# Optimization experiments

Measured on AMD Instinct MI355X. Metric: run time of the kernel, lower is better.

Reference implementation:

```python
import jax, jax.numpy as jnp
import numpy as np

C_RADIUS = 20.0  # weighted-L1 ball radius from the cvxpy constraint
EPS = 1e-30


def weighted_l1_ball_projection(q, w, c):
    """Euclidean projection of each row of q onto {x : sum_i w_i*|x_i| <= c}, w>=0.
    Closed-form via sorted breakpoints: x_i = sign(q_i)*max(|q_i| - lam*w_i, 0).
    q, w: [B, D].
    """
    aq = jnp.abs(q)
    wa = w * aq                               # w_i |q_i|
    feasible = jnp.sum(wa, axis=-1) <= c      # already inside the ball
    # breakpoint ratios; coords with w==0 are never clipped -> push to the end
    r = jnp.where(w > 0, aq / jnp.maximum(w, EPS), -jnp.inf)
    order = jnp.argsort(-r, axis=-1)
    wa_s = jnp.take_along_axis(wa, order, axis=-1)
    w2_s = jnp.take_along_axis(w * w, order, axis=-1)
    r_s = jnp.take_along_axis(r, order, axis=-1)
    A = jnp.cumsum(wa_s, axis=-1)             # prefix sums over candidate active sets
    B = jnp.cumsum(w2_s, axis=-1)
    lam_k = (A - c) / jnp.maximum(B, EPS)
    valid = r_s > lam_k                       # active-set condition
    k = jnp.sum(valid, axis=-1)               # size of true active set
    idx = jnp.maximum(k - 1, 0)
    lam = jnp.take_along_axis(lam_k, idx[:, None], axis=-1)[:, 0]
    lam = jnp.where(feasible, 0.0, jnp.maximum(lam, 0.0))
    return jnp.sign(q) * jnp.maximum(aq - lam[:, None] * w, 0.0)


def setup_inputs() -> dict:
    key = jax.random.key(0)
    ks = jax.random.split(key, 8)
    state_dim, action_dim, B = 17, 6, 262144
    # scale state so the weighted-L1 constraint is occasionally active
    state = 4.0 * jax.random.normal(ks[0], (B, state_dim), dtype=jnp.float32)
    def lin(kw, kb, fan_out, fan_in):
        bound = 1.0 / np.sqrt(fan_in)
        W = jax.random.uniform(kw, (fan_out, fan_in), jnp.float32, -bound, bound)
        b = jax.random.uniform(kb, (fan_out,), jnp.float32, -bound, bound)
        return W, b
    l1_w, l1_b = lin(ks[1], ks[2], 400, state_dim)
    l2_w, l2_b = lin(ks[3], ks[4], 300, 400)
    l3_w, l3_b = lin(ks[5], ks[6], action_dim, 300)
    return {"state": state, "l1_w": l1_w, "l1_b": l1_b, "l2_w": l2_w,
            "l2_b": l2_b, "l3_w": l3_w, "l3_b": l3_b, "training": 0}


def reference(state, l1_w, l1_b, l2_w, l2_b, l3_w, l3_b, training):
    max_action = 1.0
    a = jax.nn.relu(state @ l1_w.T + l1_b)
    a = jax.nn.relu(a @ l2_w.T + l2_b)
    scaled_a = max_action * jnp.tanh(a @ l3_w.T + l3_b)  # [B, 6]
    # IS_TRAINING path: QP  min 0.5||x||^2 - q^T x  s.t. sum |x_i * s[11+i]| <= 20
    w = jnp.abs(state[:, 11:17])
    return weighted_l1_ball_projection(scaled_a, w, C_RADIUS)
```

## Files before the change

### kernel.cpp

```cpp
#include <hip/hip_runtime.h>
#include <math.h>

typedef _Float16 half2v __attribute__((ext_vector_type(2)));
typedef __fp16 fp16x2 __attribute__((ext_vector_type(2)));
typedef _Float16 half4 __attribute__((ext_vector_type(4)));
typedef _Float16 half8 __attribute__((ext_vector_type(8)));
typedef float floatx4 __attribute__((ext_vector_type(4)));

#define C_RADIUS 20.0f


__global__ void actor_prep(const float* __restrict__ w1, const float* __restrict__ b1,
                           const float* __restrict__ w2, const float* __restrict__ b2,
                           const float* __restrict__ w3, const float* __restrict__ b3,
                           _Float16* __restrict__ ws) {
  int gid = blockIdx.x * 256 + threadIdx.x;
  if (gid >= 19072) return;
  half8 hv;
  _Float16* dst;
  if (gid < 1792) {
    int l = gid & 63, tn = gid >> 6;
    int n = tn * 16 + (l & 15);
    int kc = 8 * (l >> 4);
#pragma unroll
    for (int e = 0; e < 8; ++e) {
      int k = kc + e;
      float v = 0.f;
      if (n < 400) {
        if (k == 0) v = b1[n];
        else if (k <= 17) v = w1[n * 17 + (k - 1)];
      }
      hv[e] = (_Float16)v;
    }
    dst = ws + gid * 8;
  } else if (gid < 1792 + 16640) {
    int g = gid - 1792;
    int l = g & 63, t = g >> 6;
    int ks = t % 13, tn = t / 13;
    int n = tn * 16 + (l & 15);
    int kc = ks * 32 + 8 * (l >> 4);
#pragma unroll
    for (int e = 0; e < 8; ++e) {
      int k = kc + e;
      float v = 0.f;
      if (n < 300) {
        if (k < 400) v = w2[n * 400 + k];
        else if (k == 400) v = b2[n];
      }
      hv[e] = (_Float16)v;
    }
    dst = ws + 14336 + g * 8;
  } else {
    int g = gid - 1792 - 16640;
    int l = g & 63, ks = g >> 6;
    int n = l & 15;
    int kc = ks * 32 + 8 * (l >> 4);
#pragma unroll
    for (int e = 0; e < 8; ++e) {
      int k = kc + e;
      float v = 0.f;
      if (n < 6) {
        if (k < 300) v = w3[n * 300 + k];
        else if (k == 300) v = b3[n];
      }
      hv[e] = (_Float16)v;
    }
    dst = ws + 147456 + g * 8;
  }
  *reinterpret_cast<half8*>(dst) = hv;
}

#define LD1 408
#define LD2 328

#define MFMA32(A, B, C) C = __builtin_amdgcn_mfma_f32_16x16x32_f16(A, B, C, 0, 0, 0)

__device__ __forceinline__ half4 pack4(float v0, float v1, float v2, float v3) {
  fp16x2 a = __builtin_amdgcn_cvt_pkrtz(v0, v1);
  fp16x2 b = __builtin_amdgcn_cvt_pkrtz(v2, v3);
  half2v a2 = __builtin_bit_cast(half2v, a);
  half2v b2 = __builtin_bit_cast(half2v, b);
  return __builtin_shufflevector(a2, b2, 0, 1, 2, 3);
}

__device__ __forceinline__ float fast_tanh(float x) {
  float e = __expf(2.0f * x);
  return 1.0f - 2.0f / (e + 1.0f);
}

__global__ __launch_bounds__(512, 6) void actor_fused(const float* __restrict__ state,
                                                      const _Float16* __restrict__ ws,
                                                      float* __restrict__ out) {
  __shared__ __align__(16) _Float16 aL[64 * LD1 + 16];

  const int tid = threadIdx.x;
  const int lane = tid & 63;
  const int w = tid >> 6;
  const int r15 = lane & 15;
  const int c4 = lane >> 4;
  const int row0 = blockIdx.x * 64;

  for (int i = tid; i < 2048; i += 512) {
    int r = i >> 5, c = i & 31;
    float v = 0.f;
    if (c == 0) v = 1.0f;
    else if (c <= 17) v = state[(row0 + r) * 17 + (c - 1)];
    aL[r * LD1 + c] = (_Float16)v;
  }
  {
    int r = tid >> 3, c = tid & 7;
    aL[r * LD1 + 400 + c] = (c == 0) ? (_Float16)1.0f : (_Float16)0.0f;
  }
  if (tid < 16) aL[64 * LD1 + tid] = (_Float16)0.0f;
  __syncthreads();

  half8 S[4];
#pragma unroll
  for (int m = 0; m < 4; ++m)
    S[m] = *reinterpret_cast<const half8*>(&aL[(16 * m + r15) * LD1 + 8 * c4]);
  __syncthreads();

  {
    const half8* W1f = reinterpret_cast<const half8*>(ws);
#pragma unroll
    for (int t = 0; t < 4; ++t) {
      int tn = w + 8 * t;
      if (tn < 25) {
        half8 aW = W1f[tn * 64 + lane];
        floatx4 acc[4];
#pragma unroll
        for (int m = 0; m < 4; ++m) {
          acc[m] = (floatx4){0.f, 0.f, 0.f, 0.f};
          MFMA32(aW, S[m], acc[m]);
        }
        int n0 = tn * 16 + 4 * c4;
#pragma unroll
        for (int m = 0; m < 4; ++m) {
          half4 hv = pack4(fmaxf(acc[m][0], 0.f), fmaxf(acc[m][1], 0.f),
                           fmaxf(acc[m][2], 0.f), fmaxf(acc[m][3], 0.f));
          *reinterpret_cast<half4*>(&aL[(16 * m + r15) * LD1 + n0]) = hv;
        }
      }
    }
  }
  __syncthreads();

  {
    const half8* W2f = reinterpret_cast<const half8*>(ws + 14336);
    const int nt = (w < 4) ? 3 : 2;
    const int tn0 = (w < 4) ? (w * 3) : (12 + (w - 4) * 2);
    floatx4 acc[4][3];
#pragma unroll
    for (int m = 0; m < 4; ++m)
#pragma unroll
      for (int t = 0; t < 3; ++t) acc[m][t] = (floatx4){0.f, 0.f, 0.f, 0.f};

    half8 bA[3];
#pragma unroll
    for (int t = 0; t < 3; ++t)
      if (t < nt) bA[t] = W2f[((tn0 + t) * 13 + 0) * 64 + lane];

#pragma unroll 1
    for (int ks = 0; ks < 13; ++ks) {
      half8 F[4];
#pragma unroll
      for (int m = 0; m < 4; ++m)
        F[m] = *reinterpret_cast<const half8*>(&aL[(16 * m + r15) * LD1 + ks * 32 + 8 * c4]);
#pragma unroll
      for (int t = 0; t < 3; ++t)
        if (t < nt)
#pragma unroll
          for (int m = 0; m < 4; ++m)
            MFMA32(bA[t], F[m], acc[m][t]);
      if (ks < 12) {
#pragma unroll
        for (int t = 0; t < 3; ++t)
          if (t < nt) bA[t] = W2f[((tn0 + t) * 13 + ks + 1) * 64 + lane];
      }
    }

    __syncthreads();

#pragma unroll
    for (int t = 0; t < 3; ++t)
      if (t < nt) {
        int n0 = (tn0 + t) * 16 + 4 * c4;
#pragma unroll
        for (int m = 0; m < 4; ++m) {
          float v0 = fmaxf(acc[m][t][0], 0.f), v1 = fmaxf(acc[m][t][1], 0.f);
          float v2 = fmaxf(acc[m][t][2], 0.f), v3 = fmaxf(acc[m][t][3], 0.f);
          if (n0 == 300) v0 = 1.0f;
          half4 hv = pack4(v0, v1, v2, v3);
          *reinterpret_cast<half4*>(&aL[(16 * m + r15) * LD2 + n0]) = hv;
        }
      }
  }
  __syncthreads();

  if (w < 4) {
    const half8* W3f = reinterpret_cast<const half8*>(ws + 147456);
    floatx4 za = (floatx4){0.f, 0.f, 0.f, 0.f};
    floatx4 zb = (floatx4){0.f, 0.f, 0.f, 0.f};
    const int row = 16 * w + r15;
#pragma unroll
    for (int ks = 0; ks < 10; ks += 2) {
      half8 F0 = *reinterpret_cast<const half8*>(&aL[row * LD2 + ks * 32 + 8 * c4]);
      half8 F1 = *reinterpret_cast<const half8*>(&aL[row * LD2 + (ks + 1) * 32 + 8 * c4]);
      MFMA32(W3f[ks * 64 + lane], F0, za);
      MFMA32(W3f[(ks + 1) * 64 + lane], F1, zb);
    }
    floatx4 z = za + zb;
    float v4 = __shfl(z[0], r15 + 16, 64);
    float v5 = __shfl(z[1], r15 + 16, 64);
    if (c4 == 0) {
      const int grow = row0 + row;
      float q[6], wv[6], aq[6], wa[6];
      q[0] = fast_tanh(z[0]); q[1] = fast_tanh(z[1]);
      q[2] = fast_tanh(z[2]); q[3] = fast_tanh(z[3]);
      q[4] = fast_tanh(v4);   q[5] = fast_tanh(v5);
      float S2 = 0.f;
#pragma unroll
      for (int i = 0; i < 6; ++i) {
        wv[i] = fabsf(state[grow * 17 + 11 + i]);
        aq[i] = fabsf(q[i]);
        wa[i] = wv[i] * aq[i];
        S2 += wa[i];
      }
      float lam = 0.f;
      if (!(S2 <= C_RADIUS)) {
        float rr[6], w2s[6], was[6];
#pragma unroll
        for (int i = 0; i < 6; ++i) {
          rr[i] = (wv[i] > 0.f) ? (aq[i] / fmaxf(wv[i], 1e-30f)) : -__builtin_inff();
          w2s[i] = wv[i] * wv[i];
          was[i] = wa[i];
        }
#pragma unroll
        for (int p = 0; p < 5; ++p)
#pragma unroll
          for (int j2 = 0; j2 < 5; ++j2)
            if (j2 < 5 - p) {
              if (rr[j2] < rr[j2 + 1]) {
                float t0 = rr[j2];  rr[j2] = rr[j2 + 1];  rr[j2 + 1] = t0;
                float t1 = w2s[j2]; w2s[j2] = w2s[j2 + 1]; w2s[j2 + 1] = t1;
                float t2 = was[j2]; was[j2] = was[j2 + 1]; was[j2 + 1] = t2;
              }
            }
        float A = 0.f, Bc = 0.f;
        float lamk[6];
        int kc = 0;
#pragma unroll
        for (int i = 0; i < 6; ++i) {
          A += was[i];
          Bc += w2s[i];
          lamk[i] = (A - C_RADIUS) / fmaxf(Bc, 1e-30f);
          if (rr[i] > lamk[i]) ++kc;
        }
        int idx = kc - 1;
        if (idx < 0) idx = 0;
        float lsel = lamk[0];
#pragma unroll
        for (int i = 1; i < 6; ++i)
          if (i == idx) lsel = lamk[i];
        lam = fmaxf(lsel, 0.f);
      }
#pragma unroll
      for (int i = 0; i < 6; ++i) {
        float x = fmaxf(aq[i] - lam * wv[i], 0.f);
        out[grow * 6 + i] = copysignf(x, q[i]);
      }
    }
  }
}

extern "C" void kernel_launch(void* const* d_in, const int* in_sizes, int n_in,
                              void* d_out, int out_size, void* d_ws, size_t ws_size,
                              hipStream_t stream) {
  const float* state = (const float*)d_in[0];
  const float* w1 = (const float*)d_in[1];
  const float* b1 = (const float*)d_in[2];
  const float* w2 = (const float*)d_in[3];
  const float* b2 = (const float*)d_in[4];
  const float* w3 = (const float*)d_in[5];
  const float* b3 = (const float*)d_in[6];
  _Float16* ws = (_Float16*)d_ws;
  float* out = (float*)d_out;

  actor_prep<<<75, 256, 0, stream>>>(w1, b1, w2, b2, w3, b3, ws);
  actor_fused<<<4096, 512, 0, stream>>>(state, ws, out);
}
```

Measured before the change: 92.96 us.

## Rebalance layer-2 MFMA work across waves and apply ReLU on packed halves

Layer 2 was split as 3 or 2 column tiles per wave over all 64 rows, which left waves 4-7 with less work. Now each wave handles 5 column tiles over half of the rows (32), so all eight waves issue the same number of MFMAs. This halves the per-wave LDS fragment reads but doubles the weight fragments each wave loads from global memory across the two row halves. The ReLU is also applied after fp16 packing with a packed max instead of four scalar fmaxf calls.

```diff
diff --git a/kernel.cpp b/kernel.cpp
--- a/kernel.cpp
+++ b/kernel.cpp
@@ -83,6 +83,11 @@
   return __builtin_shufflevector(a2, b2, 0, 1, 2, 3);
 }
 
+__device__ __forceinline__ half4 pack4_relu(floatx4 v) {
+  half4 hv = pack4(v[0], v[1], v[2], v[3]);
+  return __builtin_elementwise_max(hv, (half4)(_Float16)0.0f);
+}
+
 __device__ __forceinline__ float fast_tanh(float x) {
   float e = __expf(2.0f * x);
   return 1.0f - 2.0f / (e + 1.0f);
@@ -136,8 +141,7 @@
         int n0 = tn * 16 + 4 * c4;
 #pragma unroll
         for (int m = 0; m < 4; ++m) {
-          half4 hv = pack4(fmaxf(acc[m][0], 0.f), fmaxf(acc[m][1], 0.f),
-                           fmaxf(acc[m][2], 0.f), fmaxf(acc[m][3], 0.f));
+          half4 hv = pack4_relu(acc[m]);
           *reinterpret_cast<half4*>(&aL[(16 * m + r15) * LD1 + n0]) = hv;
         }
       }
@@ -147,53 +151,45 @@
 
   {
     const half8* W2f = reinterpret_cast<const half8*>(ws + 14336);
-    const int nt = (w < 4) ? 3 : 2;
-    const int tn0 = (w < 4) ? (w * 3) : (12 + (w - 4) * 2);
-    floatx4 acc[4][3];
-#pragma unroll
-    for (int m = 0; m < 4; ++m)
-#pragma unroll
-      for (int t = 0; t < 3; ++t) acc[m][t] = (floatx4){0.f, 0.f, 0.f, 0.f};
-
-    half8 bA[3];
-#pragma unroll
-    for (int t = 0; t < 3; ++t)
-      if (t < nt) bA[t] = W2f[((tn0 + t) * 13 + 0) * 64 + lane];
+    const int mh = w >> 2;
+    const int tnb = (w & 3) * 5;
+    floatx4 acc[2][5];
+#pragma unroll
+    for (int mi = 0; mi < 2; ++mi)
+#pragma unroll
+      for (int t = 0; t < 5; ++t) acc[mi][t] = (floatx4){0.f, 0.f, 0.f, 0.f};
+
+    half8 bA[5];
+#pragma unroll
+    for (int t = 0; t < 5; ++t) bA[t] = W2f[((tnb + t) * 13 + 0) * 64 + lane];
 
 #pragma unroll 1
     for (int ks = 0; ks < 13; ++ks) {
-      half8 F[4];
-#pragma unroll
-      for (int m = 0; m < 4; ++m)
-        F[m] = *reinterpret_cast<const half8*>(&aL[(16 * m + r15) * LD1 + ks * 32 + 8 * c4]);
-#pragma unroll
-      for (int t = 0; t < 3; ++t)
-        if (t < nt)
-#pragma unroll
-          for (int m = 0; m < 4; ++m)
-            MFMA32(bA[t], F[m], acc[m][t]);
+      half8 F0 = *reinterpret_cast<const half8*>(&aL[(32 * mh + r15) * LD1 + ks * 32 + 8 * c4]);
+      half8 F1 = *reinterpret_cast<const half8*>(&aL[(32 * mh + 16 + r15) * LD1 + ks * 32 + 8 * c4]);
+#pragma unroll
+      for (int t = 0; t < 5; ++t) {
+        MFMA32(bA[t], F0, acc[0][t]);
+        MFMA32(bA[t], F1, acc[1][t]);
+      }
       if (ks < 12) {
 #pragma unroll
-        for (int t = 0; t < 3; ++t)
-          if (t < nt) bA[t] = W2f[((tn0 + t) * 13 + ks + 1) * 64 + lane];
+        for (int t = 0; t < 5; ++t) bA[t] = W2f[((tnb + t) * 13 + ks + 1) * 64 + lane];
       }
     }
 
     __syncthreads();
 
 #pragma unroll
-    for (int t = 0; t < 3; ++t)
-      if (t < nt) {
-        int n0 = (tn0 + t) * 16 + 4 * c4;
-#pragma unroll
-        for (int m = 0; m < 4; ++m) {
-          float v0 = fmaxf(acc[m][t][0], 0.f), v1 = fmaxf(acc[m][t][1], 0.f);
-          float v2 = fmaxf(acc[m][t][2], 0.f), v3 = fmaxf(acc[m][t][3], 0.f);
-          if (n0 == 300) v0 = 1.0f;
-          half4 hv = pack4(v0, v1, v2, v3);
-          *reinterpret_cast<half4*>(&aL[(16 * m + r15) * LD2 + n0]) = hv;
-        }
-      }
+    for (int t = 0; t < 5; ++t) {
+      int n0 = (tnb + t) * 16 + 4 * c4;
+#pragma unroll
+      for (int mi = 0; mi < 2; ++mi) {
+        half4 hv = pack4_relu(acc[mi][t]);
+        if (n0 == 300) hv[0] = (_Float16)1.0f;
+        *reinterpret_cast<half4*>(&aL[(32 * mh + 16 * mi + r15) * LD2 + n0]) = hv;
+      }
+    }
   }
   __syncthreads();
 
```

Measured after the change: 101.6 us. 1.09x slower.

## XOR-swizzle LDS activation layout and fuse ReLU into packed fp16 max

Applied to the files above, without the earlier changes.

Replaces the padded row strides of the shared-memory activation buffer with power-of-two-aligned strides plus an XOR swizzle of 16-byte chunks keyed on row, applied to every write and read of layer activations. The aim is to cut LDS bank conflicts on the half8 fragment loads and the half4 stores. ReLU is now applied after fp16 packing with a vector max instead of four scalar fmaxf calls. The change raises LDS usage slightly, and the swizzle has to stay consistent across every access path, including the bias columns.

```diff
diff --git a/kernel.cpp b/kernel.cpp
--- a/kernel.cpp
+++ b/kernel.cpp
@@ -70,8 +70,8 @@
   *reinterpret_cast<half8*>(dst) = hv;
 }
 
-#define LD1 408
-#define LD2 328
+#define LD1 416
+#define LD2 352
 
 #define MFMA32(A, B, C) C = __builtin_amdgcn_mfma_f32_16x16x32_f16(A, B, C, 0, 0, 0)
 
@@ -83,6 +83,11 @@
   return __builtin_shufflevector(a2, b2, 0, 1, 2, 3);
 }
 
+__device__ __forceinline__ half4 pack4_relu(floatx4 v) {
+  half4 hv = pack4(v[0], v[1], v[2], v[3]);
+  return __builtin_elementwise_max(hv, (half4)(_Float16)0.0f);
+}
+
 __device__ __forceinline__ float fast_tanh(float x) {
   float e = __expf(2.0f * x);
   return 1.0f - 2.0f / (e + 1.0f);
@@ -91,13 +96,14 @@
 __global__ __launch_bounds__(512, 6) void actor_fused(const float* __restrict__ state,
                                                       const _Float16* __restrict__ ws,
                                                       float* __restrict__ out) {
-  __shared__ __align__(16) _Float16 aL[64 * LD1 + 16];
+  __shared__ __align__(16) _Float16 aL[64 * LD1];
 
   const int tid = threadIdx.x;
   const int lane = tid & 63;
   const int w = tid >> 6;
   const int r15 = lane & 15;
   const int c4 = lane >> 4;
+  const int rx = r15 & 3;
   const int row0 = blockIdx.x * 64;
 
   for (int i = tid; i < 2048; i += 512) {
@@ -105,19 +111,19 @@
     float v = 0.f;
     if (c == 0) v = 1.0f;
     else if (c <= 17) v = state[(row0 + r) * 17 + (c - 1)];
-    aL[r * LD1 + c] = (_Float16)v;
-  }
-  {
-    int r = tid >> 3, c = tid & 7;
-    aL[r * LD1 + 400 + c] = (c == 0) ? (_Float16)1.0f : (_Float16)0.0f;
-  }
-  if (tid < 16) aL[64 * LD1 + tid] = (_Float16)0.0f;
+    aL[r * LD1 + ((((c >> 3) ^ (r & 3))) << 3) + (c & 7)] = (_Float16)v;
+  }
+  for (int i = tid; i < 1024; i += 512) {
+    int r = i >> 4, c = 400 + (i & 15);
+    aL[r * LD1 + ((((c >> 3) ^ (r & 3))) << 3) + (c & 7)] =
+        (c == 400) ? (_Float16)1.0f : (_Float16)0.0f;
+  }
   __syncthreads();
 
   half8 S[4];
 #pragma unroll
   for (int m = 0; m < 4; ++m)
-    S[m] = *reinterpret_cast<const half8*>(&aL[(16 * m + r15) * LD1 + 8 * c4]);
+    S[m] = *reinterpret_cast<const half8*>(&aL[(16 * m + r15) * LD1 + ((c4 ^ rx) << 3)]);
   __syncthreads();
 
   {
@@ -133,12 +139,12 @@
           acc[m] = (floatx4){0.f, 0.f, 0.f, 0.f};
           MFMA32(aW, S[m], acc[m]);
         }
-        int n0 = tn * 16 + 4 * c4;
+        int ch = ((tn << 1) + (c4 >> 1)) ^ rx;
+        int eo = (ch << 3) + ((c4 & 1) << 2);
 #pragma unroll
         for (int m = 0; m < 4; ++m) {
-          half4 hv = pack4(fmaxf(acc[m][0], 0.f), fmaxf(acc[m][1], 0.f),
-                           fmaxf(acc[m][2], 0.f), fmaxf(acc[m][3], 0.f));
-          *reinterpret_cast<half4*>(&aL[(16 * m + r15) * LD1 + n0]) = hv;
+          half4 hv = pack4_relu(acc[m]);
+          *reinterpret_cast<half4*>(&aL[(16 * m + r15) * LD1 + eo]) = hv;
         }
       }
     }
@@ -160,12 +166,13 @@
     for (int t = 0; t < 3; ++t)
       if (t < nt) bA[t] = W2f[((tn0 + t) * 13 + 0) * 64 + lane];
 
+    const int fco = (c4 ^ rx) << 3;
 #pragma unroll 1
     for (int ks = 0; ks < 13; ++ks) {
       half8 F[4];
 #pragma unroll
       for (int m = 0; m < 4; ++m)
-        F[m] = *reinterpret_cast<const half8*>(&aL[(16 * m + r15) * LD1 + ks * 32 + 8 * c4]);
+        F[m] = *reinterpret_cast<const half8*>(&aL[(16 * m + r15) * LD1 + ks * 32 + fco]);
 #pragma unroll
       for (int t = 0; t < 3; ++t)
         if (t < nt)
@@ -185,13 +192,13 @@
     for (int t = 0; t < 3; ++t)
       if (t < nt) {
         int n0 = (tn0 + t) * 16 + 4 * c4;
+        int ch = (((tn0 + t) << 1) + (c4 >> 1)) ^ rx;
+        int eo = (ch << 3) + ((c4 & 1) << 2);
 #pragma unroll
         for (int m = 0; m < 4; ++m) {
-          float v0 = fmaxf(acc[m][t][0], 0.f), v1 = fmaxf(acc[m][t][1], 0.f);
-          float v2 = fmaxf(acc[m][t][2], 0.f), v3 = fmaxf(acc[m][t][3], 0.f);
-          if (n0 == 300) v0 = 1.0f;
-          half4 hv = pack4(v0, v1, v2, v3);
-          *reinterpret_cast<half4*>(&aL[(16 * m + r15) * LD2 + n0]) = hv;
+          half4 hv = pack4_relu(acc[m][t]);
+          if (n0 == 300) hv[0] = (_Float16)1.0f;
+          *reinterpret_cast<half4*>(&aL[(16 * m + r15) * LD2 + eo]) = hv;
         }
       }
   }
@@ -202,10 +209,11 @@
     floatx4 za = (floatx4){0.f, 0.f, 0.f, 0.f};
     floatx4 zb = (floatx4){0.f, 0.f, 0.f, 0.f};
     const int row = 16 * w + r15;
+    const int fco = (c4 ^ rx) << 3;
 #pragma unroll
     for (int ks = 0; ks < 10; ks += 2) {
-      half8 F0 = *reinterpret_cast<const half8*>(&aL[row * LD2 + ks * 32 + 8 * c4]);
-      half8 F1 = *reinterpret_cast<const half8*>(&aL[row * LD2 + (ks + 1) * 32 + 8 * c4]);
+      half8 F0 = *reinterpret_cast<const half8*>(&aL[row * LD2 + ks * 32 + fco]);
+      half8 F1 = *reinterpret_cast<const half8*>(&aL[row * LD2 + (ks + 1) * 32 + fco]);
       MFMA32(W3f[ks * 64 + lane], F0, za);
       MFMA32(W3f[(ks + 1) * 64 + lane], F1, zb);
     }
```

After: 93.99 us. Within noise of the previous version (+1.1%).

## Load state directly into MFMA fragments, pack-then-relu in fp16, add setprio

Applied to the files above, without the earlier changes.

Layer-1 input fragments are now built directly from global state in registers instead of being staged through shared memory, which removes the staging loop and two barriers. ReLU is applied after packing to fp16 with a vector max, replacing four scalar fmaxf per fragment. The layer-2 MFMA block is wrapped in s_setprio to favour issuing matrix instructions. Global loads in the direct path are uncoalesced per-lane scalar reads of 17-float rows.

```diff
diff --git a/kernel.cpp b/kernel.cpp
--- a/kernel.cpp
+++ b/kernel.cpp
@@ -83,6 +83,11 @@
   return __builtin_shufflevector(a2, b2, 0, 1, 2, 3);
 }
 
+__device__ __forceinline__ half4 pack4_relu(floatx4 v) {
+  half4 hv = pack4(v[0], v[1], v[2], v[3]);
+  return __builtin_elementwise_max(hv, (half4)(_Float16)0.0f);
+}
+
 __device__ __forceinline__ float fast_tanh(float x) {
   float e = __expf(2.0f * x);
   return 1.0f - 2.0f / (e + 1.0f);
@@ -100,25 +105,30 @@
   const int c4 = lane >> 4;
   const int row0 = blockIdx.x * 64;
 
-  for (int i = tid; i < 2048; i += 512) {
-    int r = i >> 5, c = i & 31;
-    float v = 0.f;
-    if (c == 0) v = 1.0f;
-    else if (c <= 17) v = state[(row0 + r) * 17 + (c - 1)];
-    aL[r * LD1 + c] = (_Float16)v;
-  }
   {
     int r = tid >> 3, c = tid & 7;
     aL[r * LD1 + 400 + c] = (c == 0) ? (_Float16)1.0f : (_Float16)0.0f;
   }
   if (tid < 16) aL[64 * LD1 + tid] = (_Float16)0.0f;
-  __syncthreads();
 
   half8 S[4];
 #pragma unroll
-  for (int m = 0; m < 4; ++m)
-    S[m] = *reinterpret_cast<const half8*>(&aL[(16 * m + r15) * LD1 + 8 * c4]);
-  __syncthreads();
+  for (int m = 0; m < 4; ++m) {
+    const float* sp = state + (size_t)(row0 + 16 * m + r15) * 17;
+    half8 v = {};
+    if (c4 == 0) {
+      v[0] = (_Float16)1.0f;
+#pragma unroll
+      for (int e = 1; e < 8; ++e) v[e] = (_Float16)sp[e - 1];
+    } else if (c4 == 1) {
+#pragma unroll
+      for (int e = 0; e < 8; ++e) v[e] = (_Float16)sp[7 + e];
+    } else if (c4 == 2) {
+      v[0] = (_Float16)sp[15];
+      v[1] = (_Float16)sp[16];
+    }
+    S[m] = v;
+  }
 
   {
     const half8* W1f = reinterpret_cast<const half8*>(ws);
@@ -136,8 +146,7 @@
         int n0 = tn * 16 + 4 * c4;
 #pragma unroll
         for (int m = 0; m < 4; ++m) {
-          half4 hv = pack4(fmaxf(acc[m][0], 0.f), fmaxf(acc[m][1], 0.f),
-                           fmaxf(acc[m][2], 0.f), fmaxf(acc[m][3], 0.f));
+          half4 hv = pack4_relu(acc[m]);
           *reinterpret_cast<half4*>(&aL[(16 * m + r15) * LD1 + n0]) = hv;
         }
       }
@@ -166,12 +175,14 @@
 #pragma unroll
       for (int m = 0; m < 4; ++m)
         F[m] = *reinterpret_cast<const half8*>(&aL[(16 * m + r15) * LD1 + ks * 32 + 8 * c4]);
+      __builtin_amdgcn_s_setprio(1);
 #pragma unroll
       for (int t = 0; t < 3; ++t)
         if (t < nt)
 #pragma unroll
           for (int m = 0; m < 4; ++m)
             MFMA32(bA[t], F[m], acc[m][t]);
+      __builtin_amdgcn_s_setprio(0);
       if (ks < 12) {
 #pragma unroll
         for (int t = 0; t < 3; ++t)
@@ -187,10 +198,8 @@
         int n0 = (tn0 + t) * 16 + 4 * c4;
 #pragma unroll
         for (int m = 0; m < 4; ++m) {
-          float v0 = fmaxf(acc[m][t][0], 0.f), v1 = fmaxf(acc[m][t][1], 0.f);
-          float v2 = fmaxf(acc[m][t][2], 0.f), v3 = fmaxf(acc[m][t][3], 0.f);
-          if (n0 == 300) v0 = 1.0f;
-          half4 hv = pack4(v0, v1, v2, v3);
+          half4 hv = pack4_relu(acc[m][t]);
+          if (n0 == 300) hv[0] = (_Float16)1.0f;
           *reinterpret_cast<half4*>(&aL[(16 * m + r15) * LD2 + n0]) = hv;
         }
       }
```

Measured after the change: 99.45 us. 7.0% more time.
